# Kernel optimization log

Measured on AMD Instinct MI355X. Metric: run time of the kernel, lower is better.

Reference implementation:

```python
import jax, jax.numpy as jnp
import numpy as np

N = 100000
E = 1600000
IN_C = 128
HID = 128
N_FACTORS = 3
N_SKILLS = 7
NEG_SLOPE = 0.2


def setup_inputs() -> dict:
    key = jax.random.key(0)
    ks = jax.random.split(key, 16)
    inp = {
        "x": jax.random.normal(ks[0], (N, IN_C), dtype=jnp.float32),
        "edge_index": jax.random.randint(ks[1], (2, E), 0, N, dtype=jnp.int64),
        # GAT layer 1
        "W1": jax.random.normal(ks[2], (HID, IN_C), dtype=jnp.float32) * (1.0 / np.sqrt(IN_C)),
        "a_src1": jax.random.normal(ks[3], (HID,), dtype=jnp.float32) * 0.1,
        "a_dst1": jax.random.normal(ks[4], (HID,), dtype=jnp.float32) * 0.1,
        "b1": jnp.zeros((HID,), dtype=jnp.float32),
        # GAT layer 2
        "W2": jax.random.normal(ks[5], (HID, HID), dtype=jnp.float32) * (1.0 / np.sqrt(HID)),
        "a_src2": jax.random.normal(ks[6], (HID,), dtype=jnp.float32) * 0.1,
        "a_dst2": jax.random.normal(ks[7], (HID,), dtype=jnp.float32) * 0.1,
        "b2": jnp.zeros((HID,), dtype=jnp.float32),
        # classifier heads
        "Wf": jax.random.normal(ks[8], (N_FACTORS, HID), dtype=jnp.float32) * (1.0 / np.sqrt(HID)),
        "bf": jnp.zeros((N_FACTORS,), dtype=jnp.float32),
        "Ws": jax.random.normal(ks[9], (N_SKILLS, HID), dtype=jnp.float32) * (1.0 / np.sqrt(HID)),
        "bs": jnp.zeros((N_SKILLS,), dtype=jnp.float32),
    }
    return inp


def _gat_layer(x, src, dst, W, a_src, a_dst, b):
    # x: [N, Fin] -> h: [N, Fout]; single-head GATConv (PyG defaults)
    n = x.shape[0]
    h = x @ W.T
    alpha_s = h @ a_src  # [N]
    alpha_d = h @ a_dst  # [N]
    e = jax.nn.leaky_relu(alpha_s[src] + alpha_d[dst], NEG_SLOPE)  # [E']
    # segment softmax over incoming edges of each dst node
    emax = jax.ops.segment_max(e, dst, num_segments=n)
    w = jnp.exp(e - emax[dst])
    denom = jax.ops.segment_sum(w, dst, num_segments=n)
    alpha = w / denom[dst]
    out = jax.ops.segment_sum(h[src] * alpha[:, None], dst, num_segments=n)
    return out + b


def reference(x, edge_index, W1, a_src1, a_dst1, b1, W2, a_src2, a_dst2, b2, Wf, bf, Ws, bs):
    # add self loops (PyG GATConv default add_self_loops=True)
    loops = jnp.arange(N, dtype=edge_index.dtype)
    src = jnp.concatenate([edge_index[0], loops])
    dst = jnp.concatenate([edge_index[1], loops])

    h = jax.nn.relu(_gat_layer(x, src, dst, W1, a_src1, a_dst1, b1))
    h = jax.nn.relu(_gat_layer(h, src, dst, W2, a_src2, a_dst2, b2))
    # dropout inactive in eval mode
    factors = h @ Wf.T + bf
    skills = h @ Ws.T + bs
    return (factors, skills)
```

## Files before the change

kernel.cpp:

```cpp
#include <hip/hip_runtime.h>
#include <hip/hip_bf16.h>
#include <hip/hip_fp16.h>
#include <math.h>

#define EPB 8192
#define BPB 256

typedef _Float16 v8h __attribute__((ext_vector_type(8)));
typedef float v4f __attribute__((ext_vector_type(4)));

__device__ inline float sum16(float v) {
#pragma unroll
  for (int off = 1; off < 16; off <<= 1) v += __shfl_xor(v, off);
  return v;
}

__device__ inline uint4 load8h(const float* p) {
  float4 a = *(const float4*)p;
  float4 b = *(const float4*)(p + 4);
  union { __half2 h[4]; uint4 u; } pk;
  pk.h[0] = __floats2half2_rn(a.x, a.y);
  pk.h[1] = __floats2half2_rn(a.z, a.w);
  pk.h[2] = __floats2half2_rn(b.x, b.y);
  pk.h[3] = __floats2half2_rn(b.z, b.w);
  return pk.u;
}
__device__ inline uint4 load8h(const __half* p) { return *(const uint4*)p; }

__device__ inline int* scan_inc512(const int* __restrict__ btot, int NB, int t,
                                   int* sA, int* sB) {
#pragma unroll
  for (int i = t; i < 512; i += 256) sA[i] = (i < NB) ? btot[i] : 0;
  __syncthreads();
  int* src = sA;
  int* dst = sB;
  for (int off = 1; off < 512; off <<= 1) {
#pragma unroll
    for (int i = t; i < 512; i += 256) {
      int v = src[i];
      if (i >= off) v += src[i - off];
      dst[i] = v;
    }
    __syncthreads();
    int* tmp = src; src = dst; dst = tmp;
  }
  return src;
}

__device__ inline void pcount_body(const int* __restrict__ ei, int* __restrict__ btot,
                                   int* __restrict__ blkoff, int* hist,
                                   int p, int t, int nE, int n, int PB, int NB) {
  for (int i = t; i < NB; i += 256) hist[i] = 0;
  __syncthreads();
  int e0 = p * EPB;
  int e1 = min(e0 + EPB, nE);
  for (int i = e0 + t; i < e1; i += 256) {
    int d = ei[nE + i];
    if ((unsigned)d < (unsigned)n) atomicAdd(&hist[d >> 8], 1);
  }
  __syncthreads();
  for (int i = t; i < NB; i += 256) {
    int h = hist[i];
    int off = atomicAdd(&btot[i], h);
    blkoff[i * PB + p] = off;
  }
}

template <typename T>
__device__ inline void gemm_tile(uint4* Xs, uint4* Ws, int t, int row0,
                                 const T* __restrict__ X, const float* __restrict__ W,
                                 const float* __restrict__ a_src,
                                 const float* __restrict__ a_dst,
                                 __half* __restrict__ H16,
                                 float* __restrict__ as_, float* __restrict__ ad_,
                                 int nrows) {
#pragma unroll
  for (int i = 0; i < 4; ++i) {
    int idx = t + i * 256;
    int r = idx >> 4;
    int j = idx & 15;
    uint4 u = make_uint4(0u, 0u, 0u, 0u);
    if (row0 + r < nrows) u = load8h(&X[(size_t)(row0 + r) * 128 + j * 8]);
    Xs[r * 16 + (j ^ (r & 15))] = u;
  }
#pragma unroll
  for (int i = 0; i < 8; ++i) {
    int idx = t + i * 256;
    int c = idx >> 4;
    int j = idx & 15;
    Ws[c * 16 + (j ^ (c & 15))] = load8h(&W[(size_t)c * 128 + j * 8]);
  }
  __syncthreads();

  int w = t >> 6;
  int lane = t & 63;
  int li = lane & 15;
  int quad = lane >> 4;

  v4f acc[8];
#pragma unroll
  for (int ct = 0; ct < 8; ++ct) acc[ct] = (v4f){0.f, 0.f, 0.f, 0.f};

#pragma unroll
  for (int kk = 0; kk < 4; ++kk) {
    int ch = kk * 4 + quad;
    union { uint4 u; v8h h; } av;
    av.u = Xs[(w * 16 + li) * 16 + (ch ^ li)];
#pragma unroll
    for (int ct = 0; ct < 8; ++ct) {
      union { uint4 u; v8h h; } bv;
      bv.u = Ws[(ct * 16 + li) * 16 + (ch ^ li)];
      acc[ct] = __builtin_amdgcn_mfma_f32_16x16x32_f16(av.h, bv.h, acc[ct], 0, 0, 0);
    }
  }

  float asum[4] = {0.f, 0.f, 0.f, 0.f};
  float adsum[4] = {0.f, 0.f, 0.f, 0.f};
#pragma unroll
  for (int ct = 0; ct < 8; ++ct) {
    float sa = a_src[ct * 16 + li];
    float da = a_dst[ct * 16 + li];
#pragma unroll
    for (int reg = 0; reg < 4; ++reg) {
      asum[reg] = fmaf(acc[ct][reg], sa, asum[reg]);
      adsum[reg] = fmaf(acc[ct][reg], da, adsum[reg]);
    }
  }
#pragma unroll
  for (int reg = 0; reg < 4; ++reg) {
    asum[reg] = sum16(asum[reg]);
    adsum[reg] = sum16(adsum[reg]);
  }
  if (li == 0) {
#pragma unroll
    for (int reg = 0; reg < 4; ++reg) {
      int r = row0 + w * 16 + quad * 4 + reg;
      if (r < nrows) {
        as_[r] = asum[reg];
        ad_[r] = adsum[reg];
      }
    }
  }

#pragma unroll
  for (int ct = 0; ct < 8; ++ct) {
#pragma unroll
    for (int reg = 0; reg < 4; ++reg) {
      float v0 = acc[ct][reg];
      float v1 = __shfl_xor(v0, 1);
      if (!(li & 1)) {
        int r = row0 + w * 16 + quad * 4 + reg;
        if (r < nrows) {
          __half2 hh = __floats2half2_rn(v0, v1);
          *(__half2*)&H16[(size_t)r * 128 + ct * 16 + li] = hh;
        }
      }
    }
  }
}

__global__ __launch_bounds__(256) void k_fused1(const int* __restrict__ ei,
                                                int* __restrict__ btot,
                                                int* __restrict__ blkoff,
                                                int nE, int n, int PB, int NB,
                                                const float* __restrict__ X,
                                                const float* __restrict__ W,
                                                const float* __restrict__ a_src,
                                                const float* __restrict__ a_dst,
                                                __half* __restrict__ H16,
                                                float* __restrict__ as_,
                                                float* __restrict__ ad_) {
  __shared__ __align__(16) char smraw[48 * 1024];
  int t = threadIdx.x;
  if ((int)blockIdx.x < PB) {
    pcount_body(ei, btot, blkoff, (int*)smraw, blockIdx.x, t, nE, n, PB, NB);
  } else {
    uint4* Xs = (uint4*)smraw;
    uint4* Ws = (uint4*)(smraw + 16384);
    int row0 = (blockIdx.x - PB) * 64;
    gemm_tile<float>(Xs, Ws, t, row0, X, W, a_src, a_dst, H16, as_, ad_, n);
  }
}

__global__ __launch_bounds__(256) void k_linear2(const __half* __restrict__ X,
                                                 const float* __restrict__ W,
                                                 const float* __restrict__ a_src,
                                                 const float* __restrict__ a_dst,
                                                 __half* __restrict__ H16,
                                                 float* __restrict__ as_,
                                                 float* __restrict__ ad_, int nrows) {
  __shared__ __align__(16) char smraw[48 * 1024];
  uint4* Xs = (uint4*)smraw;
  uint4* Ws = (uint4*)(smraw + 16384);
  gemm_tile<__half>(Xs, Ws, threadIdx.x, blockIdx.x * 64, X, W, a_src, a_dst,
                    H16, as_, ad_, nrows);
}

__global__ __launch_bounds__(256) void k_ppart(const int* __restrict__ ei,
                                               const int* __restrict__ btot,
                                               const int* __restrict__ blkoff,
                                               unsigned* __restrict__ part,
                                               int nE, int n, int PB, int NB) {
  __shared__ int sA[512], sB[512];
  __shared__ int cur[512];
  int p = blockIdx.x, t = threadIdx.x;
  int* inc = scan_inc512(btot, NB, t, sA, sB);
  for (int i = t; i < NB; i += 256) {
    int excl = (i == 0) ? 0 : inc[i - 1];
    cur[i] = excl + blkoff[i * PB + p];
  }
  __syncthreads();
  int e0 = p * EPB;
  int e1 = min(e0 + EPB, nE);
  for (int i = e0 + t; i < e1; i += 256) {
    int d = ei[nE + i];
    int s = ei[i];
    if ((unsigned)d < (unsigned)n) {
      int pos = atomicAdd(&cur[d >> 8], 1);
      part[pos] = ((unsigned)s << 8) | (unsigned)(d & 255);
    }
  }
}

__global__ __launch_bounds__(256) void k_bucket(const unsigned* __restrict__ part,
                                                const int* __restrict__ btot,
                                                int* __restrict__ rowptr,
                                                int* __restrict__ col,
                                                int NB, int n) {
  __shared__ int sdeg[256];
  __shared__ int sscan[256];
  __shared__ int lcol[8448];
  int b = blockIdx.x, t = threadIdx.x;
  int node0 = b * BPB;
  int* inc = scan_inc512(btot, NB, t, lcol, lcol + 512);
  int ebeg = (b == 0) ? 0 : inc[b - 1];
  int eend = inc[b];
  int total = inc[NB - 1];
  __syncthreads();

  int cnt = eend - ebeg;
  if (cnt > 8192) cnt = 8192;
  int nloc = n - node0;
  if (nloc > BPB) nloc = BPB;

  sdeg[t] = (t < nloc) ? 1 : 0;
  __syncthreads();
  for (int i = t; i < cnt; i += 256) {
    int dl = part[ebeg + i] & 255u;
    atomicAdd(&sdeg[dl], 1);
  }
  __syncthreads();
  int v = sdeg[t];
  sscan[t] = v;
  __syncthreads();
  for (int off = 1; off < 256; off <<= 1) {
    int x = (t >= off) ? sscan[t - off] : 0;
    __syncthreads();
    sscan[t] += x;
    __syncthreads();
  }
  int excl = sscan[t] - v;
  int gbase = ebeg + node0;
  if (t < nloc) rowptr[node0 + t] = gbase + excl;
  if (b == NB - 1 && t == 0) rowptr[n] = total + n;
  if (t < nloc) lcol[excl] = node0 + t;
  sdeg[t] = excl + 1;
  __syncthreads();
  for (int i = t; i < cnt; i += 256) {
    unsigned e = part[ebeg + i];
    int pos = atomicAdd(&sdeg[e & 255u], 1);
    lcol[pos] = (int)(e >> 8);
  }
  __syncthreads();
  int T = cnt + nloc;
  for (int i = t; i < T; i += 256) col[gbase + i] = lcol[i];
}

#define AGG_SLOT(K, QREG)                                                  \
  if (K == 0 || jj + K < trips) {                                          \
    float wj = __shfl(wgt, gb | (jj + K));                                 \
    uint4 cur = QREG;                                                      \
    if (jj + K + 4 < trips) {                                              \
      int sq = __shfl(s, gb | (jj + K + 4));                               \
      QREG = *(const uint4*)(h + (size_t)sq * 128 + li * 8);               \
    }                                                                      \
    float2 f0 = __half22float2(*(__half2*)&cur.x);                         \
    float2 f1 = __half22float2(*(__half2*)&cur.y);                         \
    float2 f2 = __half22float2(*(__half2*)&cur.z);                         \
    float2 f3 = __half22float2(*(__half2*)&cur.w);                         \
    acc0 = fmaf(f0.x, wj, acc0); acc1 = fmaf(f0.y, wj, acc1);              \
    acc2 = fmaf(f1.x, wj, acc2); acc3 = fmaf(f1.y, wj, acc3);              \
    acc4 = fmaf(f2.x, wj, acc4); acc5 = fmaf(f2.y, wj, acc5);              \
    acc6 = fmaf(f3.x, wj, acc6); acc7 = fmaf(f3.y, wj, acc7);              \
  }

template <bool HEADS>
__global__ __launch_bounds__(256) void k_agg_t(const __half* __restrict__ h,
                                               const float* __restrict__ as_,
                                               const float* __restrict__ ad_,
                                               const int* __restrict__ rowptr,
                                               const int* __restrict__ col,
                                               const float* __restrict__ bias,
                                               void* __restrict__ outp,
                                               const float* __restrict__ Wf,
                                               const float* __restrict__ bf,
                                               const float* __restrict__ Wsk,
                                               const float* __restrict__ bs,
                                               int n) {
  int gid = blockIdx.x * 256 + threadIdx.x;
  int wid = gid >> 6;
  int lane = gid & 63;
  int g = lane >> 4;
  int li = lane & 15;
  int gb = lane & 48;
  int node = wid * 4 + g;
  bool valid = node < n;
  int beg = 0, end = 0;
  float adv = 0.f;
  if (valid) {
    beg = rowptr[node];
    end = rowptr[node + 1];
    adv = ad_[node];
  }
  int deg = end - beg;
  int md = deg;
  md = max(md, __shfl_xor(md, 16));
  md = max(md, __shfl_xor(md, 32));

  float acc0 = 0.f, acc1 = 0.f, acc2 = 0.f, acc3 = 0.f;
  float acc4 = 0.f, acc5 = 0.f, acc6 = 0.f, acc7 = 0.f;
  float den_l = 0.f;

  for (int base = 0; base < md; base += 16) {
    int s = 0;
    float wgt = 0.f;
    if (base + li < deg) {
      s = col[beg + base + li];
      if ((unsigned)s >= (unsigned)n) s = 0;
      float v = as_[s] + adv;
      v = (v > 0.f) ? v : 0.2f * v;
      wgt = __expf(v);
    }
    den_l += wgt;

    int rem = md - base;
    int trips = rem > 16 ? 16 : rem;
    uint4 q0 = make_uint4(0u, 0u, 0u, 0u);
    uint4 q1 = q0, q2 = q0, q3 = q0;
    {
      int sq = __shfl(s, gb);
      q0 = *(const uint4*)(h + (size_t)sq * 128 + li * 8);
      if (trips > 1) { sq = __shfl(s, gb | 1); q1 = *(const uint4*)(h + (size_t)sq * 128 + li * 8); }
      if (trips > 2) { sq = __shfl(s, gb | 2); q2 = *(const uint4*)(h + (size_t)sq * 128 + li * 8); }
      if (trips > 3) { sq = __shfl(s, gb | 3); q3 = *(const uint4*)(h + (size_t)sq * 128 + li * 8); }
    }
    for (int jj = 0; jj < trips; jj += 4) {
      AGG_SLOT(0, q0)
      AGG_SLOT(1, q1)
      AGG_SLOT(2, q2)
      AGG_SLOT(3, q3)
    }
  }

  float den = sum16(den_l);
  float inv = 1.0f / den;

  float4 bv0 = *(const float4*)&bias[li * 8];
  float4 bv1 = *(const float4*)&bias[li * 8 + 4];
  float o0 = fmaxf(fmaf(acc0, inv, bv0.x), 0.f);
  float o1 = fmaxf(fmaf(acc1, inv, bv0.y), 0.f);
  float o2 = fmaxf(fmaf(acc2, inv, bv0.z), 0.f);
  float o3 = fmaxf(fmaf(acc3, inv, bv0.w), 0.f);
  float o4 = fmaxf(fmaf(acc4, inv, bv1.x), 0.f);
  float o5 = fmaxf(fmaf(acc5, inv, bv1.y), 0.f);
  float o6 = fmaxf(fmaf(acc6, inv, bv1.z), 0.f);
  float o7 = fmaxf(fmaf(acc7, inv, bv1.w), 0.f);

  if (!HEADS) {
    if (valid) {
      union { __half2 h2[4]; uint4 u; } pk;
      pk.h2[0] = __floats2half2_rn(o0, o1);
      pk.h2[1] = __floats2half2_rn(o2, o3);
      pk.h2[2] = __floats2half2_rn(o4, o5);
      pk.h2[3] = __floats2half2_rn(o6, o7);
      *(uint4*)&(((__half*)outp)[(size_t)node * 128 + li * 8]) = pk.u;
    }
  } else {
    float p[10];
#pragma unroll
    for (int j = 0; j < 3; ++j) {
      float4 w0 = *(const float4*)&Wf[(size_t)j * 128 + li * 8];
      float4 w1 = *(const float4*)&Wf[(size_t)j * 128 + li * 8 + 4];
      p[j] = o0 * w0.x + o1 * w0.y + o2 * w0.z + o3 * w0.w +
             o4 * w1.x + o5 * w1.y + o6 * w1.z + o7 * w1.w;
    }
#pragma unroll
    for (int j = 0; j < 7; ++j) {
      float4 w0 = *(const float4*)&Wsk[(size_t)j * 128 + li * 8];
      float4 w1 = *(const float4*)&Wsk[(size_t)j * 128 + li * 8 + 4];
      p[3 + j] = o0 * w0.x + o1 * w0.y + o2 * w0.z + o3 * w0.w +
                 o4 * w1.x + o5 * w1.y + o6 * w1.z + o7 * w1.w;
    }
#pragma unroll
    for (int j = 0; j < 10; ++j) p[j] = sum16(p[j]);
    if (li == 0 && valid) {
      float* out = (float*)outp;
#pragma unroll
      for (int j = 0; j < 3; ++j) out[(size_t)node * 3 + j] = p[j] + bf[j];
      float* sk = out + (size_t)n * 3;
#pragma unroll
      for (int j = 0; j < 7; ++j) sk[(size_t)node * 7 + j] = p[3 + j] + bs[j];
    }
  }
}

extern "C" void kernel_launch(void* const* d_in, const int* in_sizes, int n_in,
                              void* d_out, int out_size, void* d_ws, size_t ws_size,
                              hipStream_t stream) {
  const float* x = (const float*)d_in[0];
  const int* ei = (const int*)d_in[1];
  const float* W1 = (const float*)d_in[2];
  const float* a_src1 = (const float*)d_in[3];
  const float* a_dst1 = (const float*)d_in[4];
  const float* b1 = (const float*)d_in[5];
  const float* W2 = (const float*)d_in[6];
  const float* a_src2 = (const float*)d_in[7];
  const float* a_dst2 = (const float*)d_in[8];
  const float* b2 = (const float*)d_in[9];
  const float* Wf = (const float*)d_in[10];
  const float* bf = (const float*)d_in[11];
  const float* Wsk = (const float*)d_in[12];
  const float* bs = (const float*)d_in[13];
  float* out = (float*)d_out;

  const int N = in_sizes[0] / 128;
  const int nE = in_sizes[1] / 2;
  const int NB = (N + BPB - 1) / BPB;
  const int PB = (nE + EPB - 1) / EPB;
  const int NCNT = NB * PB;

  char* w = (char*)d_ws;
  auto carve = [&](size_t bytes) {
    char* p = w;
    w += (bytes + 255) & ~(size_t)255;
    return (void*)p;
  };
  __half* H16 = (__half*)carve((size_t)N * 128 * 2);
  __half* B16 = (__half*)carve((size_t)N * 128 * 2);
  float* as_ = (float*)carve((size_t)N * 4);
  float* ad_ = (float*)carve((size_t)N * 4);
  int* rowptr = (int*)carve((size_t)(N + 1) * 4);
  int* col = (int*)carve((size_t)(nE + N) * 4);
  int* btot = (int*)carve((size_t)(NB + 1) * 4);
  int* blkoff = (int*)carve((size_t)NCNT * 4);
  unsigned* part = (unsigned*)carve((size_t)nE * 4);

  dim3 b256(256);
  const int gemm_blocks = (N + 63) / 64;
  const int agg_blocks = (((N + 3) / 4) * 64 + 255) / 256;

  hipMemsetAsync(btot, 0, (size_t)(NB + 1) * 4, stream);
  k_fused1<<<PB + gemm_blocks, b256, 0, stream>>>(ei, btot, blkoff, nE, N, PB, NB,
                                                  x, W1, a_src1, a_dst1, H16, as_, ad_);
  k_ppart<<<PB, b256, 0, stream>>>(ei, btot, blkoff, part, nE, N, PB, NB);
  k_bucket<<<NB, b256, 0, stream>>>(part, btot, rowptr, col, NB, N);

  k_agg_t<false><<<agg_blocks, b256, 0, stream>>>(H16, as_, ad_, rowptr, col, b1, B16,
                                                  nullptr, nullptr, nullptr, nullptr, N);

  k_linear2<<<gemm_blocks, b256, 0, stream>>>(B16, W2, a_src2, a_dst2, H16, as_, ad_, N);
  k_agg_t<true><<<agg_blocks, b256, 0, stream>>>(H16, as_, ad_, rowptr, col, b2, out,
                                                 Wf, bf, Wsk, bs, N);
}
```

Baseline: 341.0 us.

## Merge edge count and partition into per-block local sort, drop global offset pass

After: 326.0 us. -4.4%, faster.

```diff
diff --git a/kernel.cpp b/kernel.cpp
--- a/kernel.cpp
+++ b/kernel.cpp
@@ -27,30 +27,16 @@
 }
 __device__ inline uint4 load8h(const __half* p) { return *(const uint4*)p; }
 
-__device__ inline int* scan_inc512(const int* __restrict__ btot, int NB, int t,
-                                   int* sA, int* sB) {
-#pragma unroll
-  for (int i = t; i < 512; i += 256) sA[i] = (i < NB) ? btot[i] : 0;
-  __syncthreads();
-  int* src = sA;
-  int* dst = sB;
-  for (int off = 1; off < 512; off <<= 1) {
-#pragma unroll
-    for (int i = t; i < 512; i += 256) {
-      int v = src[i];
-      if (i >= off) v += src[i - off];
-      dst[i] = v;
-    }
-    __syncthreads();
-    int* tmp = src; src = dst; dst = tmp;
-  }
-  return src;
-}
-
-__device__ inline void pcount_body(const int* __restrict__ ei, int* __restrict__ btot,
-                                   int* __restrict__ blkoff, int* hist,
-                                   int p, int t, int nE, int n, int PB, int NB) {
-  for (int i = t; i < NB; i += 256) hist[i] = 0;
+__device__ inline void psort_body(const int* __restrict__ ei, int* __restrict__ blkoff,
+                                  unsigned* __restrict__ part, char* smraw,
+                                  int p, int t, int nE, int n, int NB) {
+  int* hist = (int*)smraw;
+  int* sA = hist + 512;
+  int* sB = sA + 512;
+  int* cur = sB + 512;
+  unsigned* buf = (unsigned*)(cur + 512);
+
+  for (int i = t; i < 512; i += 256) hist[i] = 0;
   __syncthreads();
   int e0 = p * EPB;
   int e1 = min(e0 + EPB, nE);
@@ -59,11 +45,38 @@
     if ((unsigned)d < (unsigned)n) atomicAdd(&hist[d >> 8], 1);
   }
   __syncthreads();
+  for (int i = t; i < 512; i += 256) sA[i] = hist[i];
+  __syncthreads();
+  int* src = sA;
+  int* dst = sB;
+  for (int off = 1; off < 512; off <<= 1) {
+    for (int i = t; i < 512; i += 256) {
+      int v = src[i];
+      if (i >= off) v += src[i - off];
+      dst[i] = v;
+    }
+    __syncthreads();
+    int* tmp = src; src = dst; dst = tmp;
+  }
+  int* bo = blkoff + (size_t)p * (NB + 1);
   for (int i = t; i < NB; i += 256) {
-    int h = hist[i];
-    int off = atomicAdd(&btot[i], h);
-    blkoff[i * PB + p] = off;
-  }
+    int excl = (i == 0) ? 0 : src[i - 1];
+    bo[i] = excl;
+    cur[i] = excl;
+  }
+  if (t == 0) bo[NB] = src[NB - 1];
+  __syncthreads();
+  for (int i = e0 + t; i < e1; i += 256) {
+    int d = ei[nE + i];
+    int s = ei[i];
+    if ((unsigned)d < (unsigned)n) {
+      int pos = atomicAdd(&cur[d >> 8], 1);
+      buf[pos] = ((unsigned)s << 8) | (unsigned)(d & 255);
+    }
+  }
+  __syncthreads();
+  int cnt = src[NB - 1];
+  for (int i = t; i < cnt; i += 256) part[e0 + i] = buf[i];
 }
 
 template <typename T>
@@ -160,8 +173,8 @@
 }
 
 __global__ __launch_bounds__(256) void k_fused1(const int* __restrict__ ei,
-                                                int* __restrict__ btot,
                                                 int* __restrict__ blkoff,
+                                                unsigned* __restrict__ part,
                                                 int nE, int n, int PB, int NB,
                                                 const float* __restrict__ X,
                                                 const float* __restrict__ W,
@@ -173,7 +186,7 @@
   __shared__ __align__(16) char smraw[48 * 1024];
   int t = threadIdx.x;
   if ((int)blockIdx.x < PB) {
-    pcount_body(ei, btot, blkoff, (int*)smraw, blockIdx.x, t, nE, n, PB, NB);
+    psort_body(ei, blkoff, part, smraw, blockIdx.x, t, nE, n, NB);
   } else {
     uint4* Xs = (uint4*)smraw;
     uint4* Ws = (uint4*)(smraw + 16384);
@@ -196,58 +209,53 @@
                     H16, as_, ad_, nrows);
 }
 
-__global__ __launch_bounds__(256) void k_ppart(const int* __restrict__ ei,
-                                               const int* __restrict__ btot,
-                                               const int* __restrict__ blkoff,
-                                               unsigned* __restrict__ part,
-                                               int nE, int n, int PB, int NB) {
-  __shared__ int sA[512], sB[512];
-  __shared__ int cur[512];
-  int p = blockIdx.x, t = threadIdx.x;
-  int* inc = scan_inc512(btot, NB, t, sA, sB);
-  for (int i = t; i < NB; i += 256) {
-    int excl = (i == 0) ? 0 : inc[i - 1];
-    cur[i] = excl + blkoff[i * PB + p];
-  }
-  __syncthreads();
-  int e0 = p * EPB;
-  int e1 = min(e0 + EPB, nE);
-  for (int i = e0 + t; i < e1; i += 256) {
-    int d = ei[nE + i];
-    int s = ei[i];
-    if ((unsigned)d < (unsigned)n) {
-      int pos = atomicAdd(&cur[d >> 8], 1);
-      part[pos] = ((unsigned)s << 8) | (unsigned)(d & 255);
-    }
-  }
-}
-
 __global__ __launch_bounds__(256) void k_bucket(const unsigned* __restrict__ part,
-                                                const int* __restrict__ btot,
+                                                const int* __restrict__ blkoff,
                                                 int* __restrict__ rowptr,
                                                 int* __restrict__ col,
-                                                int NB, int n) {
+                                                int PB, int NB, int n) {
   __shared__ int sdeg[256];
   __shared__ int sscan[256];
+  __shared__ int pbeg[256];
+  __shared__ int pend[256];
+  __shared__ int red[256];
   __shared__ int lcol[8448];
   int b = blockIdx.x, t = threadIdx.x;
   int node0 = b * BPB;
-  int* inc = scan_inc512(btot, NB, t, lcol, lcol + 512);
-  int ebeg = (b == 0) ? 0 : inc[b - 1];
-  int eend = inc[b];
-  int total = inc[NB - 1];
-  __syncthreads();
-
-  int cnt = eend - ebeg;
+
+  int lb = 0, le = 0;
+  if (t < PB) {
+    lb = blkoff[(size_t)t * (NB + 1) + b];
+    le = blkoff[(size_t)t * (NB + 1) + b + 1];
+  }
+  pbeg[t] = lb;
+  pend[t] = le;
+  red[t] = lb;
+  __syncthreads();
+  for (int off = 128; off; off >>= 1) {
+    if (t < off) red[t] += red[t + off];
+    __syncthreads();
+  }
+  int ebeg = red[0];
+  __syncthreads();
+  red[t] = le - lb;
+  __syncthreads();
+  for (int off = 128; off; off >>= 1) {
+    if (t < off) red[t] += red[t + off];
+    __syncthreads();
+  }
+  int cnt = red[0];
+  __syncthreads();
   if (cnt > 8192) cnt = 8192;
+
   int nloc = n - node0;
   if (nloc > BPB) nloc = BPB;
 
   sdeg[t] = (t < nloc) ? 1 : 0;
   __syncthreads();
-  for (int i = t; i < cnt; i += 256) {
-    int dl = part[ebeg + i] & 255u;
-    atomicAdd(&sdeg[dl], 1);
+  if (t < PB) {
+    const unsigned* base = part + (size_t)t * EPB;
+    for (int j = pbeg[t]; j < pend[t]; ++j) atomicAdd(&sdeg[base[j] & 255u], 1);
   }
   __syncthreads();
   int v = sdeg[t];
@@ -262,14 +270,17 @@
   int excl = sscan[t] - v;
   int gbase = ebeg + node0;
   if (t < nloc) rowptr[node0 + t] = gbase + excl;
-  if (b == NB - 1 && t == 0) rowptr[n] = total + n;
+  if (b == NB - 1 && t == 0) rowptr[n] = ebeg + cnt + n;
   if (t < nloc) lcol[excl] = node0 + t;
   sdeg[t] = excl + 1;
   __syncthreads();
-  for (int i = t; i < cnt; i += 256) {
-    unsigned e = part[ebeg + i];
-    int pos = atomicAdd(&sdeg[e & 255u], 1);
-    lcol[pos] = (int)(e >> 8);
+  if (t < PB) {
+    const unsigned* base = part + (size_t)t * EPB;
+    for (int j = pbeg[t]; j < pend[t]; ++j) {
+      unsigned e = base[j];
+      int pos = atomicAdd(&sdeg[e & 255u], 1);
+      lcol[pos] = (int)(e >> 8);
+    }
   }
   __syncthreads();
   int T = cnt + nloc;
@@ -437,7 +448,6 @@
   const int nE = in_sizes[1] / 2;
   const int NB = (N + BPB - 1) / BPB;
   const int PB = (nE + EPB - 1) / EPB;
-  const int NCNT = NB * PB;
 
   char* w = (char*)d_ws;
   auto carve = [&](size_t bytes) {
@@ -451,19 +461,16 @@
   float* ad_ = (float*)carve((size_t)N * 4);
   int* rowptr = (int*)carve((size_t)(N + 1) * 4);
   int* col = (int*)carve((size_t)(nE + N) * 4);
-  int* btot = (int*)carve((size_t)(NB + 1) * 4);
-  int* blkoff = (int*)carve((size_t)NCNT * 4);
+  int* blkoff = (int*)carve((size_t)PB * (NB + 1) * 4);
   unsigned* part = (unsigned*)carve((size_t)nE * 4);
 
   dim3 b256(256);
   const int gemm_blocks = (N + 63) / 64;
   const int agg_blocks = (((N + 3) / 4) * 64 + 255) / 256;
 
-  hipMemsetAsync(btot, 0, (size_t)(NB + 1) * 4, stream);
-  k_fused1<<<PB + gemm_blocks, b256, 0, stream>>>(ei, btot, blkoff, nE, N, PB, NB,
+  k_fused1<<<PB + gemm_blocks, b256, 0, stream>>>(ei, blkoff, part, nE, N, PB, NB,
                                                   x, W1, a_src1, a_dst1, H16, as_, ad_);
-  k_ppart<<<PB, b256, 0, stream>>>(ei, btot, blkoff, part, nE, N, PB, NB);
-  k_bucket<<<NB, b256, 0, stream>>>(part, btot, rowptr, col, NB, N);
+  k_bucket<<<NB, b256, 0, stream>>>(part, blkoff, rowptr, col, PB, NB, N);
 
   k_agg_t<false><<<agg_blocks, b256, 0, stream>>>(H16, as_, ad_, rowptr, col, b1, B16,
                                                   nullptr, nullptr, nullptr, nullptr, N);
```
